# Kernel tuning notes

Measured on AMD Instinct MI355X. Metric: run time of the kernel, lower is better.

Reference implementation:

```python
import jax, jax.numpy as jnp
import numpy as np

EPS = 1e-5
N_LANG = 5

def _ln(x, gamma, beta):
    mu = jnp.mean(x, axis=-1, keepdims=True)
    var = jnp.mean((x - mu) ** 2, axis=-1, keepdims=True)
    return (x - mu) * jax.lax.rsqrt(var + EPS) * gamma + beta

def setup_inputs() -> dict:
    key = jax.random.key(0)
    ks = jax.random.split(key, 20)
    B, S, E, T, H = 16, 512, 768, 768, 1024
    s = lambda fan_in: 1.0 / np.sqrt(fan_in)
    inp = {
        'ner_features': jax.random.normal(ks[0], (B, S, E), jnp.float32),
        'topic_features': jax.random.normal(ks[1], (B, S, T), jnp.float32),
        'language_ids': jax.random.randint(ks[2], (B,), 0, N_LANG, jnp.int64),
        # ner transform: Linear(E,H) + LayerNorm(H)
        'W_ner': jax.random.uniform(ks[3], (E, H), jnp.float32, -s(E), s(E)),
        'b_ner': jnp.zeros((H,), jnp.float32),
        'g_ner': jnp.ones((H,), jnp.float32),
        'be_ner': jnp.zeros((H,), jnp.float32),
        # topic transform: Linear(T,H) + LayerNorm(H)
        'W_top': jax.random.uniform(ks[4], (T, H), jnp.float32, -s(T), s(T)),
        'b_top': jnp.zeros((H,), jnp.float32),
        'g_top': jnp.ones((H,), jnp.float32),
        'be_top': jnp.zeros((H,), jnp.float32),
        # 5 language gate networks, stacked on leading lang axis
        'Wg1': jax.random.uniform(ks[5], (N_LANG, 2 * H, H), jnp.float32, -s(2 * H), s(2 * H)),
        'bg1': jnp.zeros((N_LANG, H), jnp.float32),
        'gg': jnp.ones((N_LANG, H), jnp.float32),
        'bg': jnp.zeros((N_LANG, H), jnp.float32),
        'Wg2': jax.random.uniform(ks[6], (N_LANG, H, 2), jnp.float32, -s(H), s(H)),
        'bg2': jnp.zeros((N_LANG, 2), jnp.float32),
    }
    return inp

def reference(ner_features, topic_features, language_ids,
              W_ner, b_ner, g_ner, be_ner,
              W_top, b_top, g_top, be_top,
              Wg1, bg1, gg, bg, Wg2, bg2):
    # shared transforms: [B,S,H]
    ner_t = jax.nn.relu(_ln(ner_features @ W_ner + b_ner, g_ner, be_ner))
    top_t = jax.nn.relu(_ln(topic_features @ W_top + b_top, g_top, be_top))
    combined = jnp.concatenate([ner_t, top_t], axis=-1)  # [B,S,2H]
    # all-language gate MLPs (faithful to the original redundant compute)
    h = jnp.einsum('bsd,ldh->lbsh', combined, Wg1) + bg1[:, None, None, :]
    h = jax.nn.relu(_ln(h, gg[:, None, None, :], bg[:, None, None, :]))
    gates_all = jax.nn.sigmoid(jnp.einsum('lbsh,lhk->lbsk', h, Wg2) + bg2[:, None, None, :])  # [L,B,S,2]
    mask = (language_ids[None, :] == jnp.arange(N_LANG)[:, None]).astype(gates_all.dtype)  # [L,B]
    gates = jnp.einsum('lb,lbsk->bsk', mask, gates_all)  # [B,S,2]
    gated_ner = ner_t * gates[..., 0:1]
    gated_topic = top_t * gates[..., 1:2]
    # dropout in eval mode (identity) for determinism
    return gated_ner, gated_topic
```

## Files before the change

### kernel.cpp

```cpp
#include <hip/hip_runtime.h>

typedef __attribute__((ext_vector_type(8))) short short8;
typedef __attribute__((ext_vector_type(4))) float f32x4;

__device__ __forceinline__ float bf2f(unsigned short u) {
    union { unsigned int i; float f; } v; v.i = ((unsigned int)u) << 16; return v.f;
}
__device__ __forceinline__ unsigned short f2bf(float f) {
    union { float f; unsigned int i; } v; v.f = f;
    unsigned int r = v.i + 0x7fffu + ((v.i >> 16) & 1u);
    return (unsigned short)(r >> 16);
}
__device__ __forceinline__ void gload16(const unsigned short* g, unsigned short* l) {
    __builtin_amdgcn_global_load_lds(
        (const __attribute__((address_space(1))) unsigned int*)g,
        (__attribute__((address_space(3))) unsigned int*)l, 16, 0, 0);
}

template<int K, int MODE>
__global__ __launch_bounds__(512, 4) void gemm_w8(
    const unsigned short* __restrict__ A,
    const unsigned short* __restrict__ Bta,
    const unsigned short* __restrict__ Btb,
    const float* __restrict__ biasa,
    const float* __restrict__ biasb,
    unsigned short* __restrict__ Cb,
    const int* __restrict__ lang)
{
    __shared__ __align__(16) unsigned short As0[128][64], Bs0[128][64];
    __shared__ __align__(16) unsigned short As1[128][64], Bs1[128][64];

    const int t = threadIdx.x;
    const int nx = gridDim.x;
    const int bid = blockIdx.y * nx + blockIdx.x;
    const int cpx = (nx * gridDim.y) >> 3;
    const int swz = (bid & 7) * cpx + (bid >> 3);
    const int gm0 = (swz >> 3) * 128;
    const int gn0 = (swz & 7) * 128;

    const unsigned short* Bt;
    const float* bias;
    int sel = 0;
    if (MODE == 0) {
        sel = gm0 >> 13;
        Bt = sel ? Btb : Bta;
        bias = sel ? biasb : biasa;
    } else {
        const int l = lang[gm0 >> 9];
        Bt = Bta + (size_t)l * ((size_t)K * 1024);
        bias = biasa + l * 1024;
    }

    const int lane = t & 63;
    const int w = t >> 6;
    const int wm = w >> 2, wn = w & 3;
    const int fr = lane & 15, g4 = lane >> 4, f7 = lane & 7;
    const int csw0 = ((0 + g4) ^ f7) * 8;
    const int csw1 = ((4 + g4) ^ f7) * 8;

    const int srow = t >> 3;
    const int swcol = ((t & 7) ^ (srow & 7)) * 8;
    const int lcol = (t & 7) * 8;
    const unsigned short* ag = A  + (size_t)(gm0 + srow) * K + swcol;
    const unsigned short* bg = Bt + (size_t)(gn0 + srow) * K + swcol;

    f32x4 acc[4][2];
#pragma unroll
    for (int m = 0; m < 4; ++m)
#pragma unroll
        for (int n = 0; n < 2; ++n)
            acc[m][n] = (f32x4){0.f, 0.f, 0.f, 0.f};

    auto stage = [&](unsigned short (*As)[64], unsigned short (*Bs)[64], int k0) {
#pragma unroll
        for (int i = 0; i < 2; ++i) {
            gload16(ag + (size_t)(i * 64) * K + k0, &As[i * 64 + srow][lcol]);
            gload16(bg + (size_t)(i * 64) * K + k0, &Bs[i * 64 + srow][lcol]);
        }
    };
    auto compute = [&](const unsigned short (*As)[64], const unsigned short (*Bs)[64]) {
        short8 a0[4], b0[2];
#pragma unroll
        for (int m = 0; m < 4; ++m) a0[m] = *(const short8*)&As[wm * 64 + m * 16 + fr][csw0];
#pragma unroll
        for (int n = 0; n < 2; ++n) b0[n] = *(const short8*)&Bs[wn * 32 + n * 16 + fr][csw0];
        __builtin_amdgcn_s_setprio(1);
#pragma unroll
        for (int m = 0; m < 4; ++m)
#pragma unroll
            for (int n = 0; n < 2; ++n)
                acc[m][n] = __builtin_amdgcn_mfma_f32_16x16x32_bf16(a0[m], b0[n], acc[m][n], 0, 0, 0);
        __builtin_amdgcn_s_setprio(0);
#pragma unroll
        for (int m = 0; m < 4; ++m) a0[m] = *(const short8*)&As[wm * 64 + m * 16 + fr][csw1];
#pragma unroll
        for (int n = 0; n < 2; ++n) b0[n] = *(const short8*)&Bs[wn * 32 + n * 16 + fr][csw1];
        __builtin_amdgcn_s_setprio(1);
#pragma unroll
        for (int m = 0; m < 4; ++m)
#pragma unroll
            for (int n = 0; n < 2; ++n)
                acc[m][n] = __builtin_amdgcn_mfma_f32_16x16x32_bf16(a0[m], b0[n], acc[m][n], 0, 0, 0);
        __builtin_amdgcn_s_setprio(0);
    };

    constexpr int NT = K / 64;
    stage(As0, Bs0, 0);
    stage(As1, Bs1, 64);

    for (int tt = 0; tt < NT; tt += 2) {
        asm volatile("s_waitcnt vmcnt(4)" ::: "memory");
        __builtin_amdgcn_s_barrier();
        asm volatile("" ::: "memory");
        __builtin_amdgcn_sched_barrier(0);
        compute(As0, Bs0);
        __builtin_amdgcn_sched_barrier(0);
        __builtin_amdgcn_s_barrier();
        if (tt + 2 < NT) stage(As0, Bs0, (tt + 2) * 64);
        if (tt + 2 < NT) asm volatile("s_waitcnt vmcnt(4)" ::: "memory");
        else             asm volatile("s_waitcnt vmcnt(0)" ::: "memory");
        __builtin_amdgcn_s_barrier();
        asm volatile("" ::: "memory");
        __builtin_amdgcn_sched_barrier(0);
        compute(As1, Bs1);
        __builtin_amdgcn_sched_barrier(0);
        __builtin_amdgcn_s_barrier();
        if (tt + 3 < NT) stage(As1, Bs1, (tt + 3) * 64);
    }

    const int fq = lane >> 4;
    const size_t pitch  = (MODE == 0) ? 2048 : 1024;
    const size_t coloff = (MODE == 0) ? (size_t)sel * 1024 : 0;
    const int rbase = (MODE == 0) ? (gm0 & 8191) : gm0;
#pragma unroll
    for (int n = 0; n < 2; ++n) {
        const int col = gn0 + wn * 32 + n * 16 + fr;
        const float bv = bias[col];
#pragma unroll
        for (int m = 0; m < 4; ++m) {
            const int row0 = rbase + wm * 64 + m * 16 + fq * 4;
#pragma unroll
            for (int r = 0; r < 4; ++r)
                Cb[(size_t)(row0 + r) * pitch + coloff + col] = f2bf(acc[m][n][r] + bv);
        }
    }
}

__device__ __forceinline__ void wt_tile(
    const float* W, unsigned short* Wt, int K, int N, int bx, int by,
    float (*tile)[33], int t)
{
    const int n0 = bx * 32, k0 = by * 32;
    const int x = t & 31, y = t >> 5;
#pragma unroll
    for (int i = 0; i < 4; ++i)
        tile[y + 8 * i][x] = W[(size_t)(k0 + y + 8 * i) * N + n0 + x];
    __syncthreads();
#pragma unroll
    for (int i = 0; i < 4; ++i)
        Wt[(size_t)(n0 + y + 8 * i) * K + k0 + x] = f2bf(tile[x][y + 8 * i]);
}
__device__ __forceinline__ void conv_chunk(
    const float* in, unsigned short* out, int b, int t)
{
    const size_t i = ((size_t)b * 256 + t) * 8;
    const float4 a = ((const float4*)(in + i))[0];
    const float4 c = ((const float4*)(in + i))[1];
    ushort4 u, v;
    u.x = f2bf(a.x); u.y = f2bf(a.y); u.z = f2bf(a.z); u.w = f2bf(a.w);
    v.x = f2bf(c.x); v.y = f2bf(c.y); v.z = f2bf(c.z); v.w = f2bf(c.w);
    *(ushort4*)(out + i)     = u;
    *(ushort4*)(out + i + 4) = v;
}

__global__ __launch_bounds__(256) void prep_all(
    const float* __restrict__ W_ner, unsigned short* __restrict__ W_nert,
    const float* __restrict__ W_top, unsigned short* __restrict__ W_topt,
    const float* __restrict__ Wg1,   unsigned short* __restrict__ Wg1t,
    const float* __restrict__ ner,   const float* __restrict__ top,
    unsigned short* __restrict__ actb)
{
    __shared__ float tile[32][33];
    int b = blockIdx.x;
    const int t = threadIdx.x;
    if (b < 768)  { wt_tile(W_ner, W_nert, 768, 1024, b % 32, b / 32, tile, t); return; }
    b -= 768;
    if (b < 768)  { wt_tile(W_top, W_topt, 768, 1024, b % 32, b / 32, tile, t); return; }
    b -= 768;
    if (b < 10240) {
        const int z = b / 2048, r = b % 2048;
        wt_tile(Wg1 + (size_t)z * 2097152, Wg1t + (size_t)z * 2097152,
                2048, 1024, r % 32, r / 32, tile, t);
        return;
    }
    b -= 10240;
    if (b < 3072) { conv_chunk(ner, actb, b, t); return; }
    b -= 3072;
    conv_chunk(top, actb + 6291456, b, t);
}

__global__ __launch_bounds__(256) void ln_relu_c(
    unsigned short* __restrict__ comb,
    const float* __restrict__ gn, const float* __restrict__ bn,
    const float* __restrict__ gt, const float* __restrict__ btp)
{
    const int b = blockIdx.x, t = threadIdx.x;
    const int r = b >> 1, half = b & 1;
    unsigned short* p = comb + (size_t)r * 2048 + half * 1024 + t * 4;
    ushort4 u = *(const ushort4*)p;
    const float x0 = bf2f(u.x), x1 = bf2f(u.y), x2 = bf2f(u.z), x3 = bf2f(u.w);
    float s1 = x0 + x1 + x2 + x3;
    float s2 = x0 * x0 + x1 * x1 + x2 * x2 + x3 * x3;
#pragma unroll
    for (int off = 32; off > 0; off >>= 1) {
        s1 += __shfl_down(s1, off);
        s2 += __shfl_down(s2, off);
    }
    __shared__ float red[8];
    const int wid = t >> 6;
    if ((t & 63) == 0) { red[wid] = s1; red[4 + wid] = s2; }
    __syncthreads();
    s1 = red[0] + red[1] + red[2] + red[3];
    s2 = red[4] + red[5] + red[6] + red[7];
    const float mean = s1 * (1.0f / 1024.0f);
    const float var = fmaxf(s2 * (1.0f / 1024.0f) - mean * mean, 0.0f);
    const float rstd = rsqrtf(var + 1e-5f);
    const float* G  = half ? gt : gn;
    const float* Be = half ? btp : bn;
    const float4 g  = ((const float4*)G)[t];
    const float4 be = ((const float4*)Be)[t];
    u.x = f2bf(fmaxf((x0 - mean) * rstd * g.x + be.x, 0.0f));
    u.y = f2bf(fmaxf((x1 - mean) * rstd * g.y + be.y, 0.0f));
    u.z = f2bf(fmaxf((x2 - mean) * rstd * g.z + be.z, 0.0f));
    u.w = f2bf(fmaxf((x3 - mean) * rstd * g.w + be.w, 0.0f));
    *(ushort4*)p = u;
}

__global__ __launch_bounds__(256) void ln_gate(
    const unsigned short* __restrict__ preln, const unsigned short* __restrict__ comb,
    const float* __restrict__ gg, const float* __restrict__ bgb,
    const float* __restrict__ Wg2, const float* __restrict__ bg2,
    const int* __restrict__ lang,
    float* __restrict__ outN, float* __restrict__ outT)
{
    const int r = blockIdx.x, t = threadIdx.x;
    const int l = lang[r >> 9];
    const ushort4 u = *(const ushort4*)(preln + (size_t)r * 1024 + t * 4);
    const float x0 = bf2f(u.x), x1 = bf2f(u.y), x2 = bf2f(u.z), x3 = bf2f(u.w);
    float s1 = x0 + x1 + x2 + x3;
    float s2 = x0 * x0 + x1 * x1 + x2 * x2 + x3 * x3;
#pragma unroll
    for (int off = 32; off > 0; off >>= 1) {
        s1 += __shfl_down(s1, off);
        s2 += __shfl_down(s2, off);
    }
    __shared__ float red[8];
    const int wid = t >> 6;
    if ((t & 63) == 0) { red[wid] = s1; red[4 + wid] = s2; }
    __syncthreads();
    s1 = red[0] + red[1] + red[2] + red[3];
    s2 = red[4] + red[5] + red[6] + red[7];
    const float mean = s1 * (1.0f / 1024.0f);
    const float var = fmaxf(s2 * (1.0f / 1024.0f) - mean * mean, 0.0f);
    const float rstd = rsqrtf(var + 1e-5f);
    const float4 g  = ((const float4*)(gg + l * 1024))[t];
    const float4 be = ((const float4*)(bgb + l * 1024))[t];
    const float h0 = fmaxf((x0 - mean) * rstd * g.x + be.x, 0.0f);
    const float h1 = fmaxf((x1 - mean) * rstd * g.y + be.y, 0.0f);
    const float h2 = fmaxf((x2 - mean) * rstd * g.z + be.z, 0.0f);
    const float h3 = fmaxf((x3 - mean) * rstd * g.w + be.w, 0.0f);
    const float4* W = (const float4*)(Wg2 + (size_t)l * 2048);
    const float4 wa = W[t * 2], wb = W[t * 2 + 1];
    float d0 = h0 * wa.x + h1 * wa.z + h2 * wb.x + h3 * wb.z;
    float d1 = h0 * wa.y + h1 * wa.w + h2 * wb.y + h3 * wb.w;
#pragma unroll
    for (int off = 32; off > 0; off >>= 1) {
        d0 += __shfl_down(d0, off);
        d1 += __shfl_down(d1, off);
    }
    __syncthreads();
    if ((t & 63) == 0) { red[wid] = d0; red[4 + wid] = d1; }
    __syncthreads();
    d0 = red[0] + red[1] + red[2] + red[3] + bg2[l * 2 + 0];
    d1 = red[4] + red[5] + red[6] + red[7] + bg2[l * 2 + 1];
    const float g0 = 1.0f / (1.0f + __expf(-d0));
    const float g1 = 1.0f / (1.0f + __expf(-d1));
    const ushort4 cn = *(const ushort4*)(comb + (size_t)r * 2048 + t * 4);
    const ushort4 ct = *(const ushort4*)(comb + (size_t)r * 2048 + 1024 + t * 4);
    float4 a, b;
    a.x = bf2f(cn.x) * g0; a.y = bf2f(cn.y) * g0; a.z = bf2f(cn.z) * g0; a.w = bf2f(cn.w) * g0;
    b.x = bf2f(ct.x) * g1; b.y = bf2f(ct.y) * g1; b.z = bf2f(ct.z) * g1; b.w = bf2f(ct.w) * g1;
    ((float4*)(outN + (size_t)r * 1024))[t] = a;
    ((float4*)(outT + (size_t)r * 1024))[t] = b;
}

extern "C" void kernel_launch(void* const* d_in, const int* in_sizes, int n_in,
                              void* d_out, int out_size, void* d_ws, size_t ws_size,
                              hipStream_t stream)
{
    const float* ner    = (const float*)d_in[0];
    const float* top    = (const float*)d_in[1];
    const int*   lang   = (const int*)d_in[2];
    const float* W_ner  = (const float*)d_in[3];
    const float* b_ner  = (const float*)d_in[4];
    const float* g_ner  = (const float*)d_in[5];
    const float* be_ner = (const float*)d_in[6];
    const float* W_top  = (const float*)d_in[7];
    const float* b_top  = (const float*)d_in[8];
    const float* g_top  = (const float*)d_in[9];
    const float* be_top = (const float*)d_in[10];
    const float* Wg1    = (const float*)d_in[11];
    const float* bg1    = (const float*)d_in[12];
    const float* gg     = (const float*)d_in[13];
    const float* bgb    = (const float*)d_in[14];
    const float* Wg2    = (const float*)d_in[15];
    const float* bg2    = (const float*)d_in[16];

    float* out  = (float*)d_out;
    float* outN = out;
    float* outT = out + 8388608;

    char* ws = (char*)d_ws;
    unsigned short* combined = (unsigned short*)ws;
    unsigned short* actb     = (unsigned short*)(ws + 33554432);
    unsigned short* preln2   = (unsigned short*)(ws + 33554432);
    unsigned short* Wg1t     = (unsigned short*)(ws + 58720256);
    unsigned short* W_nert   = (unsigned short*)outT;
    unsigned short* W_topt   = W_nert + 786432;

    prep_all<<<17920, 256, 0, stream>>>(W_ner, W_nert, W_top, W_topt,
                                        Wg1, Wg1t, ner, top, actb);

    gemm_w8<768, 0><<<dim3(8, 128), 512, 0, stream>>>(
        actb, W_nert, W_topt, b_ner, b_top, combined, nullptr);
    ln_relu_c<<<16384, 256, 0, stream>>>(combined, g_ner, be_ner, g_top, be_top);

    gemm_w8<2048, 1><<<dim3(8, 64), 512, 0, stream>>>(
        combined, Wg1t, nullptr, bg1, nullptr, preln2, lang);

    ln_gate<<<8192, 256, 0, stream>>>(preln2, combined, gg, bgb, Wg2, bg2, lang, outN, outT);
}
```

Baseline: 133.7 us.

## Fuse fp32-to-bf16 activation conversion into first GEMM's A-tile loading

Removes the separate conversion of the fp32 ner/topic activations to a bf16 buffer in the prep kernel. A new first GEMM reads fp32 A directly into registers, converts to bf16 and writes to LDS, while B still streams through direct global-to-LDS loads, all in a reworked double-buffered pipeline. This avoids writing and re-reading about 25 MB of intermediate bf16 activations. The cost is doubled A-side global read bytes inside the GEMM, plus extra register pressure and conversion ALU work in the main loop.

```diff
diff --git a/kernel.cpp b/kernel.cpp
--- a/kernel.cpp
+++ b/kernel.cpp
@@ -16,17 +16,30 @@
         (const __attribute__((address_space(1))) unsigned int*)g,
         (__attribute__((address_space(3))) unsigned int*)l, 16, 0, 0);
 }
-
-template<int K, int MODE>
-__global__ __launch_bounds__(512, 4) void gemm_w8(
-    const unsigned short* __restrict__ A,
+__device__ __forceinline__ short8 cvt8(float4 a, float4 b) {
+    short8 s;
+    s[0] = (short)f2bf(a.x); s[1] = (short)f2bf(a.y);
+    s[2] = (short)f2bf(a.z); s[3] = (short)f2bf(a.w);
+    s[4] = (short)f2bf(b.x); s[5] = (short)f2bf(b.y);
+    s[6] = (short)f2bf(b.z); s[7] = (short)f2bf(b.w);
+    return s;
+}
+
+#define VM(n) asm volatile("s_waitcnt vmcnt(%0)" :: "i"(n) : "memory")
+#define LGK0() asm volatile("s_waitcnt lgkmcnt(0)" ::: "memory")
+#define SBAR() __builtin_amdgcn_s_barrier()
+#define SCHED0() __builtin_amdgcn_sched_barrier(0)
+
+__global__ __launch_bounds__(512, 4) void gemm_f32a(
+    const float* __restrict__ nerA, const float* __restrict__ topA,
     const unsigned short* __restrict__ Bta,
     const unsigned short* __restrict__ Btb,
     const float* __restrict__ biasa,
     const float* __restrict__ biasb,
-    unsigned short* __restrict__ Cb,
-    const int* __restrict__ lang)
-{
+    unsigned short* __restrict__ Cb)
+{
+    constexpr int K = 768;
+    constexpr int NT = K / 64;
     __shared__ __align__(16) unsigned short As0[128][64], Bs0[128][64];
     __shared__ __align__(16) unsigned short As1[128][64], Bs1[128][64];
 
@@ -38,18 +51,10 @@
     const int gm0 = (swz >> 3) * 128;
     const int gn0 = (swz & 7) * 128;
 
-    const unsigned short* Bt;
-    const float* bias;
-    int sel = 0;
-    if (MODE == 0) {
-        sel = gm0 >> 13;
-        Bt = sel ? Btb : Bta;
-        bias = sel ? biasb : biasa;
-    } else {
-        const int l = lang[gm0 >> 9];
-        Bt = Bta + (size_t)l * ((size_t)K * 1024);
-        bias = biasa + l * 1024;
-    }
+    const int sel = gm0 >> 13;
+    const unsigned short* Bt = sel ? Btb : Bta;
+    const float* bias = sel ? biasb : biasa;
+    const float* Ab = sel ? topA : nerA;
 
     const int lane = t & 63;
     const int w = t >> 6;
@@ -61,6 +66,139 @@
     const int srow = t >> 3;
     const int swcol = ((t & 7) ^ (srow & 7)) * 8;
     const int lcol = (t & 7) * 8;
+    const float* af = Ab + (size_t)((gm0 & 8191) + srow) * K + swcol;
+    const unsigned short* bg = Bt + (size_t)(gn0 + srow) * K + swcol;
+
+    f32x4 acc[4][2];
+#pragma unroll
+    for (int m = 0; m < 4; ++m)
+#pragma unroll
+        for (int n = 0; n < 2; ++n)
+            acc[m][n] = (f32x4){0.f, 0.f, 0.f, 0.f};
+
+    float4 rg0[4], rg1[4];
+
+    auto issueA = [&](float4* rg, int k0) {
+        const float4* p0 = (const float4*)(af + k0);
+        const float4* p1 = (const float4*)(af + (size_t)64 * K + k0);
+        rg[0] = p0[0]; rg[1] = p0[1];
+        rg[2] = p1[0]; rg[3] = p1[1];
+    };
+    auto writeA = [&](unsigned short (*As)[64], const float4* rg) {
+        *(short8*)&As[srow][lcol]      = cvt8(rg[0], rg[1]);
+        *(short8*)&As[64 + srow][lcol] = cvt8(rg[2], rg[3]);
+    };
+    auto gloadB = [&](unsigned short (*Bs)[64], int k0) {
+#pragma unroll
+        for (int i = 0; i < 2; ++i)
+            gload16(bg + (size_t)(i * 64) * K + k0, &Bs[i * 64 + srow][lcol]);
+    };
+    auto compute = [&](const unsigned short (*As)[64], const unsigned short (*Bs)[64]) {
+        short8 a0[4], b0[2];
+#pragma unroll
+        for (int m = 0; m < 4; ++m) a0[m] = *(const short8*)&As[wm * 64 + m * 16 + fr][csw0];
+#pragma unroll
+        for (int n = 0; n < 2; ++n) b0[n] = *(const short8*)&Bs[wn * 32 + n * 16 + fr][csw0];
+        __builtin_amdgcn_s_setprio(1);
+#pragma unroll
+        for (int m = 0; m < 4; ++m)
+#pragma unroll
+            for (int n = 0; n < 2; ++n)
+                acc[m][n] = __builtin_amdgcn_mfma_f32_16x16x32_bf16(a0[m], b0[n], acc[m][n], 0, 0, 0);
+        __builtin_amdgcn_s_setprio(0);
+#pragma unroll
+        for (int m = 0; m < 4; ++m) a0[m] = *(const short8*)&As[wm * 64 + m * 16 + fr][csw1];
+#pragma unroll
+        for (int n = 0; n < 2; ++n) b0[n] = *(const short8*)&Bs[wn * 32 + n * 16 + fr][csw1];
+        __builtin_amdgcn_s_setprio(1);
+#pragma unroll
+        for (int m = 0; m < 4; ++m)
+#pragma unroll
+            for (int n = 0; n < 2; ++n)
+                acc[m][n] = __builtin_amdgcn_mfma_f32_16x16x32_bf16(a0[m], b0[n], acc[m][n], 0, 0, 0);
+        __builtin_amdgcn_s_setprio(0);
+    };
+
+    issueA(rg0, 0);
+    gloadB(Bs0, 0);
+    issueA(rg1, 64);
+    gloadB(Bs1, 64);
+    VM(8);
+    writeA(As0, rg0);
+
+    for (int tt = 0; tt < NT; tt += 2) {
+        if (tt + 1 < NT) VM(2); else VM(0);
+        if (tt + 1 < NT) writeA(As1, rg1);
+        if (tt + 2 < NT) issueA(rg0, (tt + 2) * 64);
+        LGK0();
+        SBAR();
+        SCHED0();
+        compute(As0, Bs0);
+        SCHED0();
+        SBAR();
+        if (tt + 2 < NT) gloadB(Bs0, (tt + 2) * 64);
+        if (tt + 2 < NT) VM(2); else VM(0);
+        if (tt + 2 < NT) writeA(As0, rg0);
+        if (tt + 3 < NT) issueA(rg1, (tt + 3) * 64);
+        LGK0();
+        SBAR();
+        SCHED0();
+        compute(As1, Bs1);
+        SCHED0();
+        SBAR();
+        if (tt + 3 < NT) gloadB(Bs1, (tt + 3) * 64);
+    }
+
+    const int fq = lane >> 4;
+    const int rbase = gm0 & 8191;
+    const size_t coloff = (size_t)sel * 1024;
+#pragma unroll
+    for (int n = 0; n < 2; ++n) {
+        const int col = gn0 + wn * 32 + n * 16 + fr;
+        const float bv = bias[col];
+#pragma unroll
+        for (int m = 0; m < 4; ++m) {
+            const int row0 = rbase + wm * 64 + m * 16 + fq * 4;
+#pragma unroll
+            for (int r = 0; r < 4; ++r)
+                Cb[(size_t)(row0 + r) * 2048 + coloff + col] = f2bf(acc[m][n][r] + bv);
+        }
+    }
+}
+
+__global__ __launch_bounds__(512, 4) void gemm_w8(
+    const unsigned short* __restrict__ A,
+    const unsigned short* __restrict__ Bta,
+    const float* __restrict__ biasa,
+    unsigned short* __restrict__ Cb,
+    const int* __restrict__ lang)
+{
+    constexpr int K = 2048;
+    __shared__ __align__(16) unsigned short As0[128][64], Bs0[128][64];
+    __shared__ __align__(16) unsigned short As1[128][64], Bs1[128][64];
+
+    const int t = threadIdx.x;
+    const int nx = gridDim.x;
+    const int bid = blockIdx.y * nx + blockIdx.x;
+    const int cpx = (nx * gridDim.y) >> 3;
+    const int swz = (bid & 7) * cpx + (bid >> 3);
+    const int gm0 = (swz >> 3) * 128;
+    const int gn0 = (swz & 7) * 128;
+
+    const int l = lang[gm0 >> 9];
+    const unsigned short* Bt = Bta + (size_t)l * ((size_t)K * 1024);
+    const float* bias = biasa + l * 1024;
+
+    const int lane = t & 63;
+    const int w = t >> 6;
+    const int wm = w >> 2, wn = w & 3;
+    const int fr = lane & 15, g4 = lane >> 4, f7 = lane & 7;
+    const int csw0 = ((0 + g4) ^ f7) * 8;
+    const int csw1 = ((4 + g4) ^ f7) * 8;
+
+    const int srow = t >> 3;
+    const int swcol = ((t & 7) ^ (srow & 7)) * 8;
+    const int lcol = (t & 7) * 8;
     const unsigned short* ag = A  + (size_t)(gm0 + srow) * K + swcol;
     const unsigned short* bg = Bt + (size_t)(gn0 + srow) * K + swcol;
 
@@ -109,39 +247,35 @@
     stage(As1, Bs1, 64);
 
     for (int tt = 0; tt < NT; tt += 2) {
-        asm volatile("s_waitcnt vmcnt(4)" ::: "memory");
-        __builtin_amdgcn_s_barrier();
+        VM(4);
+        SBAR();
         asm volatile("" ::: "memory");
-        __builtin_amdgcn_sched_barrier(0);
+        SCHED0();
         compute(As0, Bs0);
-        __builtin_amdgcn_sched_barrier(0);
-        __builtin_amdgcn_s_barrier();
+        SCHED0();
+        SBAR();
         if (tt + 2 < NT) stage(As0, Bs0, (tt + 2) * 64);
-        if (tt + 2 < NT) asm volatile("s_waitcnt vmcnt(4)" ::: "memory");
-        else             asm volatile("s_waitcnt vmcnt(0)" ::: "memory");
-        __builtin_amdgcn_s_barrier();
+        if (tt + 2 < NT) VM(4); else VM(0);
+        SBAR();
         asm volatile("" ::: "memory");
-        __builtin_amdgcn_sched_barrier(0);
+        SCHED0();
         compute(As1, Bs1);
-        __builtin_amdgcn_sched_barrier(0);
-        __builtin_amdgcn_s_barrier();
+        SCHED0();
+        SBAR();
         if (tt + 3 < NT) stage(As1, Bs1, (tt + 3) * 64);
     }
 
     const int fq = lane >> 4;
-    const size_t pitch  = (MODE == 0) ? 2048 : 1024;
-    const size_t coloff = (MODE == 0) ? (size_t)sel * 1024 : 0;
-    const int rbase = (MODE == 0) ? (gm0 & 8191) : gm0;
 #pragma unroll
     for (int n = 0; n < 2; ++n) {
         const int col = gn0 + wn * 32 + n * 16 + fr;
         const float bv = bias[col];
 #pragma unroll
         for (int m = 0; m < 4; ++m) {
-            const int row0 = rbase + wm * 64 + m * 16 + fq * 4;
+            const int row0 = gm0 + wm * 64 + m * 16 + fq * 4;
 #pragma unroll
             for (int r = 0; r < 4; ++r)
-                Cb[(size_t)(row0 + r) * pitch + coloff + col] = f2bf(acc[m][n][r] + bv);
+                Cb[(size_t)(row0 + r) * 1024 + col] = f2bf(acc[m][n][r] + bv);
         }
     }
 }
@@ -160,25 +294,11 @@
     for (int i = 0; i < 4; ++i)
         Wt[(size_t)(n0 + y + 8 * i) * K + k0 + x] = f2bf(tile[x][y + 8 * i]);
 }
-__device__ __forceinline__ void conv_chunk(
-    const float* in, unsigned short* out, int b, int t)
-{
-    const size_t i = ((size_t)b * 256 + t) * 8;
-    const float4 a = ((const float4*)(in + i))[0];
-    const float4 c = ((const float4*)(in + i))[1];
-    ushort4 u, v;
-    u.x = f2bf(a.x); u.y = f2bf(a.y); u.z = f2bf(a.z); u.w = f2bf(a.w);
-    v.x = f2bf(c.x); v.y = f2bf(c.y); v.z = f2bf(c.z); v.w = f2bf(c.w);
-    *(ushort4*)(out + i)     = u;
-    *(ushort4*)(out + i + 4) = v;
-}
 
 __global__ __launch_bounds__(256) void prep_all(
     const float* __restrict__ W_ner, unsigned short* __restrict__ W_nert,
     const float* __restrict__ W_top, unsigned short* __restrict__ W_topt,
-    const float* __restrict__ Wg1,   unsigned short* __restrict__ Wg1t,
-    const float* __restrict__ ner,   const float* __restrict__ top,
-    unsigned short* __restrict__ actb)
+    const float* __restrict__ Wg1,   unsigned short* __restrict__ Wg1t)
 {
     __shared__ float tile[32][33];
     int b = blockIdx.x;
@@ -187,16 +307,9 @@
     b -= 768;
     if (b < 768)  { wt_tile(W_top, W_topt, 768, 1024, b % 32, b / 32, tile, t); return; }
     b -= 768;
-    if (b < 10240) {
-        const int z = b / 2048, r = b % 2048;
-        wt_tile(Wg1 + (size_t)z * 2097152, Wg1t + (size_t)z * 2097152,
-                2048, 1024, r % 32, r / 32, tile, t);
-        return;
-    }
-    b -= 10240;
-    if (b < 3072) { conv_chunk(ner, actb, b, t); return; }
-    b -= 3072;
-    conv_chunk(top, actb + 6291456, b, t);
+    const int z = b / 2048, r = b % 2048;
+    wt_tile(Wg1 + (size_t)z * 2097152, Wg1t + (size_t)z * 2097152,
+            2048, 1024, r % 32, r / 32, tile, t);
 }
 
 __global__ __launch_bounds__(256) void ln_relu_c(
@@ -322,21 +435,18 @@
 
     char* ws = (char*)d_ws;
     unsigned short* combined = (unsigned short*)ws;
-    unsigned short* actb     = (unsigned short*)(ws + 33554432);
     unsigned short* preln2   = (unsigned short*)(ws + 33554432);
     unsigned short* Wg1t     = (unsigned short*)(ws + 58720256);
     unsigned short* W_nert   = (unsigned short*)outT;
     unsigned short* W_topt   = W_nert + 786432;
 
-    prep_all<<<17920, 256, 0, stream>>>(W_ner, W_nert, W_top, W_topt,
-                                        Wg1, Wg1t, ner, top, actb);
-
-    gemm_w8<768, 0><<<dim3(8, 128), 512, 0, stream>>>(
-        actb, W_nert, W_topt, b_ner, b_top, combined, nullptr);
+    prep_all<<<11776, 256, 0, stream>>>(W_ner, W_nert, W_top, W_topt, Wg1, Wg1t);
+
+    gemm_f32a<<<dim3(8, 128), 512, 0, stream>>>(
+        ner, top, W_nert, W_topt, b_ner, b_top, combined);
     ln_relu_c<<<16384, 256, 0, stream>>>(combined, g_ner, be_ner, g_top, be_top);
 
-    gemm_w8<2048, 1><<<dim3(8, 64), 512, 0, stream>>>(
-        combined, Wg1t, nullptr, bg1, nullptr, preln2, lang);
+    gemm_w8<<<dim3(8, 64), 512, 0, stream>>>(combined, Wg1t, bg1, preln2, lang);
 
     ln_gate<<<8192, 256, 0, stream>>>(preln2, combined, gg, bgb, Wg2, bg2, lang, outN, outT);
 }
```

Measured after the change: 138.6 us. 3.7% more time.
